# Optimization experiments

Measured on AMD Instinct MI355X. Metric: run time of the kernel, lower is better.

## Reference

```python
import jax, jax.numpy as jnp
import numpy as np


def setup_inputs() -> dict:
    key = jax.random.key(0)
    k1, k2, k3 = jax.random.split(key, 3)
    B, N1, N2 = 2, 8192, 8192
    xyz1 = jax.random.normal(k1, (B, 3, N1), dtype=jnp.float32)
    xyz2 = jax.random.normal(k2, (B, 3, N2), dtype=jnp.float32)
    flow1 = 0.1 * jax.random.normal(k3, (B, 3, N1), dtype=jnp.float32)
    return {"xyz1": xyz1, "xyz2": xyz2, "flow1": flow1, "K": 16}


def reference(xyz1, xyz2, flow1, K):
    # PointWarping3 with initial_radius == 0 (KNN branch).
    # xyz1, xyz2, flow1: [B, 3, N]
    p1 = (xyz1 + flow1).transpose(0, 2, 1)   # xyz1_to_2, [B, N1, 3]
    p2 = xyz2.transpose(0, 2, 1)             # [B, N2, 3]
    f1 = flow1.transpose(0, 2, 1)            # [B, N1, 3]
    # pairwise squared distances [B, N2, N1]
    d2 = ((p2 * p2).sum(-1, keepdims=True)
          - 2.0 * jnp.einsum('bnc,bmc->bnm', p2, p1)
          + (p1 * p1).sum(-1)[:, None, :])
    _, idx = jax.lax.top_k(-d2, K)           # K nearest source points, [B, N2, K]
    grouped = jax.vmap(lambda f, i: f[i])(f1, idx)  # gather flows, [B, N2, K, 3]
    flow2 = grouped.mean(axis=2)             # [B, N2, 3]
    warped_xyz2 = (p2 - flow2).transpose(0, 2, 1)   # [B, 3, N2]
    return warped_xyz2
```

## Files before the change

### kernel.cpp

```cpp
#include <hip/hip_runtime.h>
#include <math.h>

#define N1 8192
#define N2 8192
#define NBATCH 2
#define KNN 16
#define QPW 4
#define NCHUNK (N1 / 64)

__global__ __launch_bounds__(256) void pw3_prep_kernel(
    const float* __restrict__ xyz1,
    const float* __restrict__ flow1,
    float4* __restrict__ p1p,
    float4* __restrict__ f1p) {
  int i = blockIdx.x * blockDim.x + threadIdx.x;
  if (i >= NBATCH * N1) return;
  int b = i >> 13;
  int m = i & (N1 - 1);
  const float* x1 = xyz1 + b * 3 * N1;
  const float* f1 = flow1 + b * 3 * N1;
  float fx = f1[m], fy = f1[N1 + m], fz = f1[2 * N1 + m];
  float px = x1[m] + fx;
  float py = x1[N1 + m] + fy;
  float pz = x1[2 * N1 + m] + fz;
  float n1 = (px * px + py * py) + pz * pz;
  p1p[i] = make_float4(px, py, pz, n1);
  f1p[i] = make_float4(fx, fy, fz, 0.0f);
}

__device__ __forceinline__ float dpp_up1_f(float x, float old_v) {
  int r = __builtin_amdgcn_update_dpp(
      __builtin_bit_cast(int, old_v), __builtin_bit_cast(int, x),
      0x111, 0xf, 0xf, false);
  return __builtin_bit_cast(float, r);
}
__device__ __forceinline__ int dpp_up1_i(int x) {
  return __builtin_amdgcn_update_dpp(0, x, 0x111, 0xf, 0xf, false);
}

__global__ __launch_bounds__(256) void pw3_knn_kernel(
    const float* __restrict__ xyz2,
    const float4* __restrict__ p1p,
    const float4* __restrict__ f1p,
    float* __restrict__ out) {
  int lane = threadIdx.x & 63;
  int sub = lane & 15;
  int mygroup = lane >> 4;
  int gwave = (int)((blockIdx.x * blockDim.x + threadIdx.x) >> 6);
  int q0 = gwave * QPW;
  int b = q0 >> 13;
  int n0 = q0 & (N2 - 1);

  const float* x2 = xyz2 + b * 3 * N2;
  float qx[QPW], qy[QPW], qz[QPW], qn[QPW];
  #pragma unroll
  for (int q = 0; q < QPW; ++q) {
    qx[q] = x2[n0 + q];
    qy[q] = x2[N2 + n0 + q];
    qz[q] = x2[2 * N2 + n0 + q];
    qn[q] = (qx[q] * qx[q] + qy[q] * qy[q]) + qz[q] * qz[q];
  }

  const float4* __restrict__ src = p1p + b * N1;

  float val = INFINITY;
  int   vidx = 0;
  float kth[QPW];
  bool  ing[QPW];
  #pragma unroll
  for (int q = 0; q < QPW; ++q) {
    kth[q] = INFINITY;
    ing[q] = (mygroup == q);
  }
  const float NEG_INF = -INFINITY;

  float4 s = src[lane];
  #pragma unroll 1
  for (int c = 0; c < NCHUNK; ++c) {
    int nc = (c + 1 < NCHUNK) ? c + 1 : NCHUNK - 1;
    float4 nx = src[nc * 64 + lane];
    int base = c * 64;

    float d[QPW];
    #pragma unroll
    for (int q = 0; q < QPW; ++q) {
      float dot = (s.x * qx[q] + s.y * qy[q]) + s.z * qz[q];
      d[q] = (qn[q] - 2.0f * dot) + s.w;
    }

    #pragma unroll
    for (int q = 0; q < QPW; ++q) {
      unsigned long long bal = __ballot(d[q] < kth[q]);
      if (bal) {
        int di = __builtin_bit_cast(int, d[q]);
        do {
          int l = __ffsll(bal) - 1;
          bal &= bal - 1;
          float cd = __builtin_bit_cast(float, __builtin_amdgcn_readlane(di, l));
          int   ci = base + l;
          float pv = dpp_up1_f(val, NEG_INF);
          int   pi = dpp_up1_i(vidx);
          bool lt  = cd < val;
          bool ltp = cd < pv;
          bool upd = ing[q] & lt;
          val  = upd ? (ltp ? pv : cd) : val;
          vidx = upd ? (ltp ? pi : ci) : vidx;
        } while (bal);
        kth[q] = __builtin_bit_cast(
            float, __builtin_amdgcn_readlane(__builtin_bit_cast(int, val),
                                             q * 16 + 15));
      }
    }
    s = nx;
  }

  float4 f = f1p[b * N1 + vidx];
  float fx = f.x, fy = f.y, fz = f.z;
  #pragma unroll
  for (int o = 8; o > 0; o >>= 1) {
    fx += __shfl_xor(fx, o);
    fy += __shfl_xor(fy, o);
    fz += __shfl_xor(fz, o);
  }

  if (sub == 0) {
    int q = mygroup;
    float ox = qx[0], oy = qy[0], oz = qz[0];
    #pragma unroll
    for (int t = 1; t < QPW; ++t) {
      if (q == t) { ox = qx[t]; oy = qy[t]; oz = qz[t]; }
    }
    int n = n0 + q;
    float* op = out + b * 3 * N2;
    const float inv_k = 1.0f / KNN;
    op[n]          = ox - fx * inv_k;
    op[N2 + n]     = oy - fy * inv_k;
    op[2 * N2 + n] = oz - fz * inv_k;
  }
}

extern "C" void kernel_launch(void* const* d_in, const int* in_sizes, int n_in,
                              void* d_out, int out_size, void* d_ws, size_t ws_size,
                              hipStream_t stream) {
  const float* xyz1  = (const float*)d_in[0];
  const float* xyz2  = (const float*)d_in[1];
  const float* flow1 = (const float*)d_in[2];
  float* out = (float*)d_out;

  float4* p1p = (float4*)d_ws;
  float4* f1p = (float4*)((char*)d_ws + (size_t)NBATCH * N1 * sizeof(float4));

  {
    int total = NBATCH * N1;
    int threads = 256;
    int blocks = (total + threads - 1) / threads;
    pw3_prep_kernel<<<blocks, threads, 0, stream>>>(xyz1, flow1, p1p, f1p);
  }
  {
    int total_waves = (NBATCH * N2) / QPW;
    int threads = 256;
    int blocks = total_waves * 64 / threads;
    pw3_knn_kernel<<<blocks, threads, 0, stream>>>(xyz2, p1p, f1p, out);
  }
}
```

Measured before the change: 106.5 us.

## Seed top-K lists with bitonic-sorted first 16 candidates to cut insertions

Before the main scan, each 16-lane group takes the distances to the first 16 source points, sorts them with a bitonic compare-exchange network built from DPP and swizzle lane exchanges, and uses the result as its initial top-K list. The K-th threshold therefore starts finite instead of infinity, which avoids the long run of serial insertions in the first chunk; those 16 already-inserted lanes are masked out for chunk 0. The per-query ballots are also computed first and OR'd together, so a chunk with no candidates for any query skips the insertion code with a single branch. The cost is a fixed sorting prologue and a few extra registers.

```diff
diff --git a/kernel.cpp b/kernel.cpp
--- a/kernel.cpp
+++ b/kernel.cpp
@@ -38,6 +38,20 @@
   return __builtin_amdgcn_update_dpp(0, x, 0x111, 0xf, 0xf, false);
 }
 
+template <int J>
+__device__ __forceinline__ int lanexor_i(int x) {
+  if constexpr (J == 1)
+    return __builtin_amdgcn_update_dpp(x, x, 0xB1, 0xf, 0xf, false);
+  else if constexpr (J == 2)
+    return __builtin_amdgcn_update_dpp(x, x, 0x4E, 0xf, 0xf, false);
+  else
+    return __builtin_amdgcn_ds_swizzle(x, (J << 10) | 0x1F);
+}
+template <int J>
+__device__ __forceinline__ float lanexor_f(float x) {
+  return __builtin_bit_cast(float, lanexor_i<J>(__builtin_bit_cast(int, x)));
+}
+
 __global__ __launch_bounds__(256) void pw3_knn_kernel(
     const float* __restrict__ xyz2,
     const float4* __restrict__ p1p,
@@ -63,18 +77,60 @@
 
   const float4* __restrict__ src = p1p + b * N1;
 
-  float val = INFINITY;
-  int   vidx = 0;
+  bool ing[QPW];
+  #pragma unroll
+  for (int q = 0; q < QPW; ++q) ing[q] = (mygroup == q);
+  const float NEG_INF = -INFINITY;
+
+  float4 s = src[lane];
+
+  float bx = __shfl(s.x, sub);
+  float by = __shfl(s.y, sub);
+  float bz = __shfl(s.z, sub);
+  float bw = __shfl(s.w, sub);
+  float di[QPW];
+  #pragma unroll
+  for (int q = 0; q < QPW; ++q) {
+    float dot = (bx * qx[q] + by * qy[q]) + bz * qz[q];
+    di[q] = (qn[q] - 2.0f * dot) + bw;
+  }
+  float dv = mygroup < 2 ? (mygroup == 0 ? di[0] : di[1])
+                         : (mygroup == 2 ? di[2] : di[3]);
+  int iv = sub;
+
+#define CE_STAGE(J, KM)                                              \
+  {                                                                  \
+    float pd = lanexor_f<J>(dv);                                     \
+    int pi = lanexor_i<J>(iv);                                       \
+    bool ms = (dv < pd) || ((dv == pd) && (iv < pi));                \
+    bool km = (((KM) >> sub) & 1) != 0;                              \
+    bool tm = (ms == km);                                            \
+    dv = tm ? dv : pd;                                               \
+    iv = tm ? iv : pi;                                               \
+  }
+  CE_STAGE(1, 0x9999u)
+  CE_STAGE(2, 0xC3C3u)
+  CE_STAGE(1, 0xA5A5u)
+  CE_STAGE(4, 0xF00Fu)
+  CE_STAGE(2, 0xCC33u)
+  CE_STAGE(1, 0xAA55u)
+  CE_STAGE(8, 0x00FFu)
+  CE_STAGE(4, 0x0F0Fu)
+  CE_STAGE(2, 0x3333u)
+  CE_STAGE(1, 0x5555u)
+#undef CE_STAGE
+
+  float val = dv;
+  int vidx = iv;
   float kth[QPW];
-  bool  ing[QPW];
-  #pragma unroll
-  for (int q = 0; q < QPW; ++q) {
-    kth[q] = INFINITY;
-    ing[q] = (mygroup == q);
-  }
-  const float NEG_INF = -INFINITY;
-
-  float4 s = src[lane];
+  #pragma unroll
+  for (int q = 0; q < QPW; ++q)
+    kth[q] = __builtin_bit_cast(
+        float, __builtin_amdgcn_readlane(__builtin_bit_cast(int, val),
+                                         q * 16 + 15));
+
+  unsigned long long excl = 0xFFFFull;
+
   #pragma unroll 1
   for (int c = 0; c < NCHUNK; ++c) {
     int nc = (c + 1 < NCHUNK) ? c + 1 : NCHUNK - 1;
@@ -88,27 +144,38 @@
       d[q] = (qn[q] - 2.0f * dot) + s.w;
     }
 
+    unsigned long long b4[QPW], orb = 0;
     #pragma unroll
     for (int q = 0; q < QPW; ++q) {
-      unsigned long long bal = __ballot(d[q] < kth[q]);
-      if (bal) {
-        int di = __builtin_bit_cast(int, d[q]);
-        do {
-          int l = __ffsll(bal) - 1;
-          bal &= bal - 1;
-          float cd = __builtin_bit_cast(float, __builtin_amdgcn_readlane(di, l));
-          int   ci = base + l;
-          float pv = dpp_up1_f(val, NEG_INF);
-          int   pi = dpp_up1_i(vidx);
-          bool lt  = cd < val;
-          bool ltp = cd < pv;
-          bool upd = ing[q] & lt;
-          val  = upd ? (ltp ? pv : cd) : val;
-          vidx = upd ? (ltp ? pi : ci) : vidx;
-        } while (bal);
-        kth[q] = __builtin_bit_cast(
-            float, __builtin_amdgcn_readlane(__builtin_bit_cast(int, val),
-                                             q * 16 + 15));
+      b4[q] = __ballot(d[q] < kth[q]) & ~excl;
+      orb |= b4[q];
+    }
+    excl = 0;
+
+    if (orb) {
+      #pragma unroll
+      for (int q = 0; q < QPW; ++q) {
+        unsigned long long bal = b4[q];
+        if (bal) {
+          int dibits = __builtin_bit_cast(int, d[q]);
+          do {
+            int l = __ffsll(bal) - 1;
+            bal &= bal - 1;
+            float cd = __builtin_bit_cast(
+                float, __builtin_amdgcn_readlane(dibits, l));
+            int ci = base + l;
+            float pv = dpp_up1_f(val, NEG_INF);
+            int pi = dpp_up1_i(vidx);
+            bool lt = cd < val;
+            bool ltp = cd < pv;
+            bool upd = ing[q] & lt;
+            val = upd ? (ltp ? pv : cd) : val;
+            vidx = upd ? (ltp ? pi : ci) : vidx;
+          } while (bal);
+          kth[q] = __builtin_bit_cast(
+              float, __builtin_amdgcn_readlane(__builtin_bit_cast(int, val),
+                                               q * 16 + 15));
+        }
       }
     }
     s = nx;
```

After: 107.1 us. Within noise of the previous version (+0.6%).
